# Kernel optimization log

Measured on AMD Instinct MI355X. Metric: run time of the kernel, lower is better.

Reference implementation:

```python
import jax, jax.numpy as jnp
import numpy as np

NEG_SLOPE = 0.2  # PyG GATConv default negative_slope


def gat_layer(x, edge_index, W, att_src, att_dst, bias):
    """GATConv with self-loops, concat heads. x:[N,F_in], W:[F_in,H*C]."""
    N = x.shape[0]
    H, C = att_src.shape
    loop = jnp.arange(N, dtype=edge_index.dtype)
    src = jnp.concatenate([edge_index[0], loop])  # [E+N]
    dst = jnp.concatenate([edge_index[1], loop])
    h = (x @ W).reshape(N, H, C)                  # [N,H,C]
    a_src = jnp.einsum('nhc,hc->nh', h, att_src)  # [N,H]
    a_dst = jnp.einsum('nhc,hc->nh', h, att_dst)
    e = a_src[src] + a_dst[dst]                   # [E+N,H]
    e = jnp.where(e > 0, e, NEG_SLOPE * e)        # leaky_relu
    # numerically-stable segment softmax over incoming edges of each dst node
    m = jax.ops.segment_max(e, dst, num_segments=N)           # [N,H]
    ex = jnp.exp(e - m[dst])
    denom = jax.ops.segment_sum(ex, dst, num_segments=N)      # [N,H]
    alpha = ex / (denom[dst] + 1e-16)                          # [E+N,H]
    out = jax.ops.segment_sum(h[src] * alpha[:, :, None], dst, num_segments=N)
    return out.reshape(N, H * C) + bias


def setup_inputs() -> dict:
    key = jax.random.key(0)
    ks = jax.random.split(key, 16)
    N, E, F_IN, HID, H, NCLS = 50000, 800000, 128, 64, 4, 40
    HC = H * HID
    s = 0.1
    return {
        'x': jax.random.normal(ks[0], (N, F_IN), jnp.float32),
        'edge_index': jax.random.randint(ks[1], (2, E), 0, N, jnp.int32),
        'W1': jax.random.normal(ks[2], (F_IN, HC), jnp.float32) * s,
        'att_src1': jax.random.normal(ks[3], (H, HID), jnp.float32) * s,
        'att_dst1': jax.random.normal(ks[4], (H, HID), jnp.float32) * s,
        'b1': jnp.zeros((HC,), jnp.float32),
        'W2': jax.random.normal(ks[5], (HC, HC), jnp.float32) * s,
        'att_src2': jax.random.normal(ks[6], (H, HID), jnp.float32) * s,
        'att_dst2': jax.random.normal(ks[7], (H, HID), jnp.float32) * s,
        'b2': jnp.zeros((HC,), jnp.float32),
        'fcW1': jax.random.normal(ks[8], (HC, HID), jnp.float32) * s,
        'fcb1': jnp.zeros((HID,), jnp.float32),
        'fcW2': jax.random.normal(ks[9], (HID, NCLS), jnp.float32) * s,
        'fcb2': jnp.zeros((NCLS,), jnp.float32),
    }


def reference(x, edge_index, W1, att_src1, att_dst1, b1,
              W2, att_src2, att_dst2, b2, fcW1, fcb1, fcW2, fcb2):
    h = gat_layer(x, edge_index, W1, att_src1, att_dst1, b1)
    h = jax.nn.elu(h)
    h = gat_layer(h, edge_index, W2, att_src2, att_dst2, b2)
    h = jax.nn.elu(h)
    h = jnp.maximum(h @ fcW1 + fcb1, 0.0)  # ReLU; dropout is identity in eval
    return h @ fcW2 + fcb2                 # [N, num_classes]
```

## Files before the change

### kernel.cpp

```cpp
#include <hip/hip_runtime.h>

typedef __attribute__((ext_vector_type(8))) _Float16 fp16x8;
typedef __attribute__((ext_vector_type(4))) float f32x4;
typedef unsigned int u32;

__device__ __forceinline__ float lrelu(float x) { return x > 0.f ? x : 0.2f * x; }
__device__ __forceinline__ float elu(float x) { return x > 0.f ? x : __expf(x) - 1.f; }

__device__ __forceinline__ void gl2lds16(const void* g, void* l) {
    __builtin_amdgcn_global_load_lds((const __attribute__((address_space(1))) u32*)g,
                                     (__attribute__((address_space(3))) u32*)l, 16, 0, 0);
}

__device__ __forceinline__ void t16t_body(const float* __restrict__ W, _Float16* __restrict__ T,
                                          int N, int Nreal, int t) {
    int lane = t & 63, rem = t >> 6;
    int kk = rem & 1; rem >>= 1;
    int ncg = N / 16;
    int cg = rem % ncg, kc = rem / ncg;
    int k = kc * 64 + kk * 32 + (lane >> 4) * 8;
    int n = cg * 16 + (lane & 15);
    fp16x8 o;
#pragma unroll
    for (int j = 0; j < 8; ++j)
        o[j] = (n < Nreal) ? (_Float16)W[(size_t)(k + j) * Nreal + n] : (_Float16)0.f;
    *(fp16x8*)(T + (size_t)t * 8) = o;
}

__global__ __launch_bounds__(256) void k_prep(const float* __restrict__ W1, _Float16* __restrict__ W1T,
                                              const float* __restrict__ W2, _Float16* __restrict__ W2T,
                                              const float* __restrict__ fcW1, _Float16* __restrict__ fWT,
                                              const float* __restrict__ fcW2, _Float16* __restrict__ f2T,
                                              const int* __restrict__ dst, int* __restrict__ cnt) {
    int b = blockIdx.x, tid = threadIdx.x;
    if (b < 16)      t16t_body(W1, W1T, 256, 256, b * 256 + tid);
    else if (b < 48) t16t_body(W2, W2T, 256, 256, (b - 16) * 256 + tid);
    else if (b < 56) t16t_body(fcW1, fWT, 64, 64, (b - 48) * 256 + tid);
    else if (b < 58) t16t_body(fcW2, f2T, 64, 40, (b - 56) * 256 + tid);
    else             atomicAdd(&cnt[dst[(b - 58) * 256 + tid]], 1);
}

__global__ __launch_bounds__(256) void k_scan_a(const int* __restrict__ cnt, int* __restrict__ s,
                                                int* __restrict__ partial, int N) {
    __shared__ int sh[256];
    int t = threadIdx.x, gid = blockIdx.x * 256 + t;
    sh[t] = gid < N ? cnt[gid] : 0;
    __syncthreads();
    for (int off = 1; off < 256; off <<= 1) {
        int add = (t >= off) ? sh[t - off] : 0;
        __syncthreads();
        sh[t] += add;
        __syncthreads();
    }
    if (gid < N) s[gid] = sh[t];
    if (t == 255) partial[blockIdx.x] = sh[255];
}
__global__ __launch_bounds__(256) void k_scan_bc(const int* __restrict__ s, const int* __restrict__ partial,
                                                 const int* __restrict__ cnt, int* __restrict__ row_ptr,
                                                 int* __restrict__ cursor, int* __restrict__ bcur, int N) {
    __shared__ int red[256];
    int t = threadIdx.x, bid = blockIdx.x;
    int a = 0;
    for (int i = t; i < bid; i += 256) a += partial[i];
    red[t] = a;
    __syncthreads();
    for (int off = 128; off; off >>= 1) {
        if (t < off) red[t] += red[t + off];
        __syncthreads();
    }
    int base = red[0];
    int gid = bid * 256 + t;
    if (gid >= N) return;
    int val = s[gid] + base;
    row_ptr[gid + 1] = val;
    int excl = val - cnt[gid];
    cursor[gid] = excl;
    if ((gid & 511) == 0) bcur[gid >> 9] = excl;
    if (gid == 0) row_ptr[0] = 0;
}

__global__ __launch_bounds__(256) void k_bin(const int* __restrict__ src, const int* __restrict__ dst,
                                             int* __restrict__ bcur, int2* __restrict__ pairbuf, int E) {
    __shared__ int cnt[128], gbase[128], excl[128], cur2[128], sh[128];
    __shared__ int saddr[1024];
    __shared__ int2 spair[1024];
    const int tid = threadIdx.x;
    const int eb = blockIdx.x * 1024;
    if (tid < 128) { cnt[tid] = 0; cur2[tid] = 0; }
    __syncthreads();
    int s_[4], d_[4];
#pragma unroll
    for (int j = 0; j < 4; ++j) {
        int e = eb + j * 256 + tid;
        if (e < E) {
            s_[j] = src[e]; d_[j] = dst[e];
            atomicAdd(&cnt[d_[j] >> 9], 1);
        } else d_[j] = -1;
    }
    __syncthreads();
    if (tid < 128) sh[tid] = cnt[tid];
    __syncthreads();
    for (int off = 1; off < 128; off <<= 1) {
        int add = 0;
        if (tid < 128 && tid >= off) add = sh[tid - off];
        __syncthreads();
        if (tid < 128) sh[tid] += add;
        __syncthreads();
    }
    if (tid < 128) {
        excl[tid] = sh[tid] - cnt[tid];
        if (cnt[tid] > 0) gbase[tid] = atomicAdd(&bcur[tid], cnt[tid]);
    }
    __syncthreads();
#pragma unroll
    for (int j = 0; j < 4; ++j) {
        if (d_[j] >= 0) {
            int b = d_[j] >> 9;
            int r = atomicAdd(&cur2[b], 1);
            int slot = excl[b] + r;
            spair[slot] = make_int2(s_[j], d_[j]);
            saddr[slot] = gbase[b] + r;
        }
    }
    __syncthreads();
    int tot = min(1024, E - eb);
#pragma unroll
    for (int j = 0; j < 4; ++j) {
        int slot = j * 256 + tid;
        if (slot < tot) pairbuf[saddr[slot]] = spair[slot];
    }
}

template<int KV, int NW, int ATT, int AFP32>
__device__ __forceinline__ void gemm_body(int bid,
              const _Float16* __restrict__ Ah, const float* __restrict__ Af,
              const _Float16* __restrict__ BT, _Float16* __restrict__ Chi,
              const float* __restrict__ att_s, const float* __restrict__ att_d,
              float* __restrict__ a_src, float* __restrict__ a_dst,
              int M, int Nc) {
    constexpr int NCG = NW / 16;
    constexpr int CHUNK = NW * 64;
    constexpr int FPW = (CHUNK / 512) / 8;
    __shared__ _Float16 Bs[CHUNK];
    const int m0 = bid * 128;
    const int tid = threadIdx.x;
    const int lane = tid & 63, wv = tid >> 6;
    const int r16 = lane & 15, quad = lane >> 4;
    const int arow = min(m0 + wv * 16 + r16, M - 1);

    f32x4 acc[NCG];
#pragma unroll
    for (int cg = 0; cg < NCG; ++cg) acc[cg] = (f32x4){0, 0, 0, 0};

    constexpr int NCH = KV / 64;
#pragma unroll
    for (int kc = 0; kc < NCH; ++kc) {
        if (kc) __syncthreads();
#pragma unroll
        for (int f = 0; f < FPW; ++f) {
            int fr = wv * FPW + f;
            gl2lds16(BT + (size_t)kc * CHUNK + fr * 512 + lane * 8, &Bs[fr * 512]);
        }
        fp16x8 ar[2];
        if (AFP32) {
            const float* Ap = Af + (size_t)arow * KV + kc * 64 + quad * 8;
#pragma unroll
            for (int kk = 0; kk < 2; ++kk) {
                float4 u0 = *(const float4*)(Ap + kk * 32);
                float4 u1 = *(const float4*)(Ap + kk * 32 + 4);
                fp16x8 h8;
                h8[0] = (_Float16)u0.x; h8[1] = (_Float16)u0.y;
                h8[2] = (_Float16)u0.z; h8[3] = (_Float16)u0.w;
                h8[4] = (_Float16)u1.x; h8[5] = (_Float16)u1.y;
                h8[6] = (_Float16)u1.z; h8[7] = (_Float16)u1.w;
                ar[kk] = h8;
            }
        } else {
            const _Float16* Ahp = Ah + (size_t)arow * KV + kc * 64 + quad * 8;
#pragma unroll
            for (int kk = 0; kk < 2; ++kk) ar[kk] = *(const fp16x8*)(Ahp + kk * 32);
        }
        __syncthreads();
#pragma unroll
        for (int kk = 0; kk < 2; ++kk) {
#pragma unroll
            for (int cg = 0; cg < NCG; ++cg) {
                fp16x8 bh = *(const fp16x8*)(&Bs[(cg * 2 + kk) * 512 + lane * 8]);
                acc[cg] = __builtin_amdgcn_mfma_f32_16x16x32_f16(ar[kk], bh, acc[cg], 0, 0, 0);
            }
        }
    }

    const int rbase = m0 + wv * 16 + quad * 4;

    if (ATT) {
#pragma unroll
        for (int hq = 0; hq < 4; ++hq) {
            float as[4], ad[4];
#pragma unroll
            for (int cg = 0; cg < 4; ++cg) {
                as[cg] = att_s[hq * 64 + cg * 16 + r16];
                ad[cg] = att_d[hq * 64 + cg * 16 + r16];
            }
#pragma unroll
            for (int i = 0; i < 4; ++i) {
                float ps = acc[hq * 4 + 0][i] * as[0] + acc[hq * 4 + 1][i] * as[1]
                         + acc[hq * 4 + 2][i] * as[2] + acc[hq * 4 + 3][i] * as[3];
                float pd = acc[hq * 4 + 0][i] * ad[0] + acc[hq * 4 + 1][i] * ad[1]
                         + acc[hq * 4 + 2][i] * ad[2] + acc[hq * 4 + 3][i] * ad[3];
#pragma unroll
                for (int d = 1; d < 16; d <<= 1) {
                    ps += __shfl_xor(ps, d);
                    pd += __shfl_xor(pd, d);
                }
                int r = rbase + i;
                if (r16 == 0 && r < M) {
                    a_src[(size_t)r * 4 + hq] = ps;
                    a_dst[(size_t)r * 4 + hq] = pd;
                }
            }
        }
    }

#pragma unroll
    for (int cg = 0; cg < NCG; ++cg) {
        int c = cg * 16 + r16;
        if (c >= Nc) continue;
#pragma unroll
        for (int i = 0; i < 4; ++i) {
            int r = rbase + i;
            if (r < M) Chi[(size_t)r * Nc + c] = (_Float16)acc[cg][i];
        }
    }
}

__global__ __launch_bounds__(512, 4)
void k_work1(const float* __restrict__ x, const _Float16* __restrict__ W1T,
             _Float16* __restrict__ h,
             const float* __restrict__ att_s, const float* __restrict__ att_d,
             float* __restrict__ a_src, float* __restrict__ a_dst,
             const int2* __restrict__ pairbuf,
             int* __restrict__ cursor, int* __restrict__ csr,
             int M, int E, int RB) {
    if ((int)blockIdx.x >= RB) {
        int base = (blockIdx.x - RB) * 2048;
#pragma unroll
        for (int j = 0; j < 4; ++j) {
            int i = base + j * 512 + threadIdx.x;
            if (i < E) {
                int2 p = pairbuf[i];
                int pos = atomicAdd(&cursor[p.y], 1);
                csr[pos] = p.x;
            }
        }
        return;
    }
    gemm_body<128, 256, 1, 1>(blockIdx.x, nullptr, x, W1T, h, att_s, att_d, a_src, a_dst, M, 256);
}

__global__ __launch_bounds__(512, 4)
void k_gemm2(const _Float16* __restrict__ Ah, const _Float16* __restrict__ BT,
             _Float16* __restrict__ h,
             const float* __restrict__ att_s, const float* __restrict__ att_d,
             float* __restrict__ a_src, float* __restrict__ a_dst, int M) {
    gemm_body<256, 256, 1, 0>(blockIdx.x, Ah, nullptr, BT, h, att_s, att_d, a_src, a_dst, M, 256);
}

__global__ __launch_bounds__(256, 4)
void k_fc(const _Float16* __restrict__ Ah, const _Float16* __restrict__ BT1,
          const _Float16* __restrict__ BT2, const float* __restrict__ b1,
          const float* __restrict__ b2, float* __restrict__ out, int M) {
    __shared__ _Float16 S[4096 + 64 * 72];
    const int m0 = blockIdx.x * 64;
    const int tid = threadIdx.x;
    const int lane = tid & 63, wv = tid >> 6;
    const int r16 = lane & 15, quad = lane >> 4;
    const int arow = min(m0 + wv * 16 + r16, M - 1);

    f32x4 acc[4];
#pragma unroll
    for (int cg = 0; cg < 4; ++cg) acc[cg] = (f32x4){0, 0, 0, 0};
#pragma unroll
    for (int kc = 0; kc < 4; ++kc) {
        if (kc) __syncthreads();
#pragma unroll
        for (int f = 0; f < 2; ++f) {
            int fr = wv * 2 + f;
            gl2lds16(BT1 + (size_t)kc * 4096 + fr * 512 + lane * 8, &S[fr * 512]);
        }
        fp16x8 ar[2];
        const _Float16* Ahp = Ah + (size_t)arow * 256 + kc * 64 + quad * 8;
#pragma unroll
        for (int kk = 0; kk < 2; ++kk) ar[kk] = *(const fp16x8*)(Ahp + kk * 32);
        __syncthreads();
#pragma unroll
        for (int kk = 0; kk < 2; ++kk) {
#pragma unroll
            for (int cg = 0; cg < 4; ++cg) {
                fp16x8 bh = *(const fp16x8*)(&S[(cg * 2 + kk) * 512 + lane * 8]);
                acc[cg] = __builtin_amdgcn_mfma_f32_16x16x32_f16(ar[kk], bh, acc[cg], 0, 0, 0);
            }
        }
    }
    __syncthreads();
    const int rloc = wv * 16 + quad * 4;
#pragma unroll
    for (int cg = 0; cg < 4; ++cg) {
        int c = cg * 16 + r16;
        float badd = b1[c];
#pragma unroll
        for (int i = 0; i < 4; ++i)
            S[4096 + (rloc + i) * 72 + c] = (_Float16)fmaxf(acc[cg][i] + badd, 0.f);
    }
    __syncthreads();
    const int arow2 = wv * 16 + r16;
    fp16x8 a2[2];
#pragma unroll
    for (int kk = 0; kk < 2; ++kk)
        a2[kk] = *(const fp16x8*)(&S[4096 + arow2 * 72 + kk * 32 + quad * 8]);
    f32x4 acc2[4];
#pragma unroll
    for (int cg = 0; cg < 4; ++cg) acc2[cg] = (f32x4){0, 0, 0, 0};
#pragma unroll
    for (int kk = 0; kk < 2; ++kk) {
#pragma unroll
        for (int cg = 0; cg < 4; ++cg) {
            fp16x8 bh = *(const fp16x8*)(BT2 + (cg * 2 + kk) * 512 + lane * 8);
            acc2[cg] = __builtin_amdgcn_mfma_f32_16x16x32_f16(a2[kk], bh, acc2[cg], 0, 0, 0);
        }
    }
    const int rbase = m0 + wv * 16 + quad * 4;
#pragma unroll
    for (int cg = 0; cg < 4; ++cg) {
        int c = cg * 16 + r16;
        if (c >= 40) continue;
        float badd = b2[c];
#pragma unroll
        for (int i = 0; i < 4; ++i) {
            int r = rbase + i;
            if (r < M) out[(size_t)r * 40 + c] = acc2[cg][i] + badd;
        }
    }
}

__global__ __launch_bounds__(256) void k_aggr8(const _Float16* __restrict__ h, const float* __restrict__ a_src,
                                               const float* __restrict__ a_dst, const int* __restrict__ row_ptr,
                                               const int* __restrict__ csr, const float* __restrict__ bias,
                                               _Float16* __restrict__ o_hi, int N) {
    int n = blockIdx.x * 8 + (threadIdx.x >> 5);
    if (n >= N) return;
    int cl = threadIdx.x & 31;
    int hd = cl >> 3;
    int beg = row_ptr[n], end = row_ptr[n + 1];
    float adh = a_dst[(size_t)4 * n + hd];
    const _Float16* hb = h + (size_t)cl * 8;

    float ws = __expf(lrelu(a_src[(size_t)4 * n + hd] + adh));
    fp16x8 sv = *(const fp16x8*)(hb + (size_t)n * 256);
    float acc[8];
#pragma unroll
    for (int j = 0; j < 8; ++j) acc[j] = ws * (float)sv[j];
    float dn = ws;

    int e = beg;
    for (; e + 4 <= end; e += 4) {
        int s0 = csr[e], s1 = csr[e + 1], s2 = csr[e + 2], s3 = csr[e + 3];
        float z0 = a_src[(size_t)4 * s0 + hd], z1 = a_src[(size_t)4 * s1 + hd];
        float z2 = a_src[(size_t)4 * s2 + hd], z3 = a_src[(size_t)4 * s3 + hd];
        fp16x8 v0 = *(const fp16x8*)(hb + (size_t)s0 * 256);
        fp16x8 v1 = *(const fp16x8*)(hb + (size_t)s1 * 256);
        fp16x8 v2 = *(const fp16x8*)(hb + (size_t)s2 * 256);
        fp16x8 v3 = *(const fp16x8*)(hb + (size_t)s3 * 256);
        float w0 = __expf(lrelu(z0 + adh)), w1 = __expf(lrelu(z1 + adh));
        float w2 = __expf(lrelu(z2 + adh)), w3 = __expf(lrelu(z3 + adh));
        dn += (w0 + w1) + (w2 + w3);
#pragma unroll
        for (int j = 0; j < 8; ++j)
            acc[j] += w0 * (float)v0[j] + w1 * (float)v1[j]
                    + w2 * (float)v2[j] + w3 * (float)v3[j];
    }
    for (; e + 2 <= end; e += 2) {
        int s0 = csr[e], s1 = csr[e + 1];
        float z0 = a_src[(size_t)4 * s0 + hd], z1 = a_src[(size_t)4 * s1 + hd];
        fp16x8 v0 = *(const fp16x8*)(hb + (size_t)s0 * 256);
        fp16x8 v1 = *(const fp16x8*)(hb + (size_t)s1 * 256);
        float w0 = __expf(lrelu(z0 + adh)), w1 = __expf(lrelu(z1 + adh));
        dn += w0 + w1;
#pragma unroll
        for (int j = 0; j < 8; ++j)
            acc[j] += w0 * (float)v0[j] + w1 * (float)v1[j];
    }
    if (e < end) {
        int s0 = csr[e];
        float w0 = __expf(lrelu(a_src[(size_t)4 * s0 + hd] + adh));
        fp16x8 v0 = *(const fp16x8*)(hb + (size_t)s0 * 256);
        dn += w0;
#pragma unroll
        for (int j = 0; j < 8; ++j) acc[j] += w0 * (float)v0[j];
    }

    float inv = 1.f / (dn + 1e-16f);
    float4 b0 = *(const float4*)(bias + cl * 8);
    float4 b1v = *(const float4*)(bias + cl * 8 + 4);
    fp16x8 hi;
    hi[0] = (_Float16)elu(acc[0] * inv + b0.x);
    hi[1] = (_Float16)elu(acc[1] * inv + b0.y);
    hi[2] = (_Float16)elu(acc[2] * inv + b0.z);
    hi[3] = (_Float16)elu(acc[3] * inv + b0.w);
    hi[4] = (_Float16)elu(acc[4] * inv + b1v.x);
    hi[5] = (_Float16)elu(acc[5] * inv + b1v.y);
    hi[6] = (_Float16)elu(acc[6] * inv + b1v.z);
    hi[7] = (_Float16)elu(acc[7] * inv + b1v.w);
    *(fp16x8*)(o_hi + (size_t)n * 256 + cl * 8) = hi;
}

extern "C" void kernel_launch(void* const* d_in, const int* in_sizes, int n_in,
                              void* d_out, int out_size, void* d_ws, size_t ws_size,
                              hipStream_t stream) {
    const int N = 50000, E = 800000, F_IN = 128, HC = 256, HID = 64, NCLS = 40;
    const float* x    = (const float*)d_in[0];
    const int*   ei   = (const int*)d_in[1];
    const float* W1   = (const float*)d_in[2];
    const float* as1  = (const float*)d_in[3];
    const float* ad1  = (const float*)d_in[4];
    const float* b1   = (const float*)d_in[5];
    const float* W2   = (const float*)d_in[6];
    const float* as2  = (const float*)d_in[7];
    const float* ad2  = (const float*)d_in[8];
    const float* b2   = (const float*)d_in[9];
    const float* fcW1 = (const float*)d_in[10];
    const float* fcb1 = (const float*)d_in[11];
    const float* fcW2 = (const float*)d_in[12];
    const float* fcb2 = (const float*)d_in[13];
    float* out = (float*)d_out;

    char* wp = (char*)d_ws;
    auto alloc = [&](size_t b) { char* p = wp; wp += (b + 255) & ~(size_t)255; return p; };
    _Float16* h     = (_Float16*)alloc((size_t)N * HC * 2);
    _Float16* ohi   = (_Float16*)alloc((size_t)N * HC * 2);
    float*  asrc  = (float*)alloc((size_t)N * 4 * 4);
    float*  adst  = (float*)alloc((size_t)N * 4 * 4);
    _Float16* W1T   = (_Float16*)alloc((size_t)F_IN * HC * 2);
    _Float16* W2T   = (_Float16*)alloc((size_t)HC * HC * 2);
    _Float16* fWT   = (_Float16*)alloc((size_t)HC * HID * 2);
    _Float16* f2T   = (_Float16*)alloc((size_t)HID * HID * 2);
    int* cnt     = (int*)alloc((size_t)N * 4);
    int* sbuf    = (int*)alloc((size_t)N * 4);
    int* part    = (int*)alloc(1024);
    int* row_ptr = (int*)alloc(((size_t)N + 1) * 4);
    int* cursor  = (int*)alloc((size_t)N * 4);
    int* csr     = (int*)alloc((size_t)E * 4);
    int* bcur    = (int*)alloc(128 * 4);
    int2* pairs  = (int2*)alloc((size_t)E * 8);

    const int* src = ei;
    const int* dst = ei + E;

    const int rb = (N + 127) / 128;
    const int node_blocks8 = (N + 7) / 8;
    const int bin_blocks = (E + 1023) / 1024;
    const int p2_blocks = (E + 2047) / 2048;
    const int fc_blocks = (N + 63) / 64;

    hipMemsetAsync(cnt, 0, (size_t)N * 4, stream);
    k_prep<<<3183, 256, 0, stream>>>(W1, W1T, W2, W2T, fcW1, fWT, fcW2, f2T, dst, cnt);
    int nb = (N + 255) / 256;
    k_scan_a<<<nb, 256, 0, stream>>>(cnt, sbuf, part, N);
    k_scan_bc<<<nb, 256, 0, stream>>>(sbuf, part, cnt, row_ptr, cursor, bcur, N);
    k_bin<<<bin_blocks, 256, 0, stream>>>(src, dst, bcur, pairs, E);
    k_work1<<<rb + p2_blocks, 512, 0, stream>>>(x, W1T, h, as1, ad1, asrc, adst,
                                                pairs, cursor, csr, N, E, rb);
    k_aggr8<<<node_blocks8, 256, 0, stream>>>(h, asrc, adst, row_ptr, csr, b1, ohi, N);
    k_gemm2<<<rb, 512, 0, stream>>>(ohi, W2T, h, as2, ad2, asrc, adst, N);
    k_aggr8<<<node_blocks8, 256, 0, stream>>>(h, asrc, adst, row_ptr, csr, b2, ohi, N);
    k_fc<<<fc_blocks, 256, 0, stream>>>(ohi, fWT, f2T, fcb1, fcb2, out, N);
}
```

Before: 340.2 us.

## Fuse layer-1 aggregation with layer-2 GEMM and attention projections

Replaces the separate layer-1 aggregation kernel and layer-2 GEMM with one kernel. Each block aggregates 16 destination nodes into an LDS tile, then runs MFMA against W2T and computes the attention logits in the same pass. This avoids writing the intermediate layer-1 output to global memory and reading it back, and removes one launch. The cost is small 16-row GEMM tiles that reload B from global/L2 per block, and no max-subtraction in the softmax. New a_src2/a_dst2 buffers are added and the h/ohi buffers swap roles.

```diff
diff --git a/kernel.cpp b/kernel.cpp
--- a/kernel.cpp
+++ b/kernel.cpp
@@ -258,12 +258,151 @@
     gemm_body<128, 256, 1, 1>(blockIdx.x, nullptr, x, W1T, h, att_s, att_d, a_src, a_dst, M, 256);
 }
 
-__global__ __launch_bounds__(512, 4)
-void k_gemm2(const _Float16* __restrict__ Ah, const _Float16* __restrict__ BT,
-             _Float16* __restrict__ h,
-             const float* __restrict__ att_s, const float* __restrict__ att_d,
-             float* __restrict__ a_src, float* __restrict__ a_dst, int M) {
-    gemm_body<256, 256, 1, 0>(blockIdx.x, Ah, nullptr, BT, h, att_s, att_d, a_src, a_dst, M, 256);
+#define AG2_LDA 264
+__global__ __launch_bounds__(512, 4) void k_ag2(
+        const _Float16* __restrict__ h, const float* __restrict__ a_src,
+        const float* __restrict__ a_dst, const int* __restrict__ row_ptr,
+        const int* __restrict__ csr, const float* __restrict__ bias,
+        const _Float16* __restrict__ BT,
+        const float* __restrict__ att_s, const float* __restrict__ att_d,
+        float* __restrict__ a_src2, float* __restrict__ a_dst2,
+        _Float16* __restrict__ h2, int N) {
+    __shared__ _Float16 A[16 * AG2_LDA];
+    __shared__ float psp[8][16], pdp[8][16];
+    const int tid = threadIdx.x;
+    const int n0 = blockIdx.x * 16;
+
+    {
+        int r = tid >> 5;
+        int n = min(n0 + r, N - 1);
+        int cl = tid & 31;
+        int hd = cl >> 3;
+        int beg = row_ptr[n], end = row_ptr[n + 1];
+        float adh = a_dst[(size_t)4 * n + hd];
+        const _Float16* hb = h + (size_t)cl * 8;
+
+        float ws = __expf(lrelu(a_src[(size_t)4 * n + hd] + adh));
+        fp16x8 sv = *(const fp16x8*)(hb + (size_t)n * 256);
+        float acc[8];
+#pragma unroll
+        for (int j = 0; j < 8; ++j) acc[j] = ws * (float)sv[j];
+        float dn = ws;
+
+        int e = beg;
+        for (; e + 4 <= end; e += 4) {
+            int s0 = csr[e], s1 = csr[e + 1], s2 = csr[e + 2], s3 = csr[e + 3];
+            float z0 = a_src[(size_t)4 * s0 + hd], z1 = a_src[(size_t)4 * s1 + hd];
+            float z2 = a_src[(size_t)4 * s2 + hd], z3 = a_src[(size_t)4 * s3 + hd];
+            fp16x8 v0 = *(const fp16x8*)(hb + (size_t)s0 * 256);
+            fp16x8 v1 = *(const fp16x8*)(hb + (size_t)s1 * 256);
+            fp16x8 v2 = *(const fp16x8*)(hb + (size_t)s2 * 256);
+            fp16x8 v3 = *(const fp16x8*)(hb + (size_t)s3 * 256);
+            float w0 = __expf(lrelu(z0 + adh)), w1 = __expf(lrelu(z1 + adh));
+            float w2 = __expf(lrelu(z2 + adh)), w3 = __expf(lrelu(z3 + adh));
+            dn += (w0 + w1) + (w2 + w3);
+#pragma unroll
+            for (int j = 0; j < 8; ++j)
+                acc[j] += w0 * (float)v0[j] + w1 * (float)v1[j]
+                        + w2 * (float)v2[j] + w3 * (float)v3[j];
+        }
+        for (; e + 2 <= end; e += 2) {
+            int s0 = csr[e], s1 = csr[e + 1];
+            float z0 = a_src[(size_t)4 * s0 + hd], z1 = a_src[(size_t)4 * s1 + hd];
+            fp16x8 v0 = *(const fp16x8*)(hb + (size_t)s0 * 256);
+            fp16x8 v1 = *(const fp16x8*)(hb + (size_t)s1 * 256);
+            float w0 = __expf(lrelu(z0 + adh)), w1 = __expf(lrelu(z1 + adh));
+            dn += w0 + w1;
+#pragma unroll
+            for (int j = 0; j < 8; ++j)
+                acc[j] += w0 * (float)v0[j] + w1 * (float)v1[j];
+        }
+        if (e < end) {
+            int s0 = csr[e];
+            float w0 = __expf(lrelu(a_src[(size_t)4 * s0 + hd] + adh));
+            fp16x8 v0 = *(const fp16x8*)(hb + (size_t)s0 * 256);
+            dn += w0;
+#pragma unroll
+            for (int j = 0; j < 8; ++j) acc[j] += w0 * (float)v0[j];
+        }
+
+        float inv = 1.f / (dn + 1e-16f);
+        float4 b0 = *(const float4*)(bias + cl * 8);
+        float4 b1v = *(const float4*)(bias + cl * 8 + 4);
+        fp16x8 hi;
+        hi[0] = (_Float16)elu(acc[0] * inv + b0.x);
+        hi[1] = (_Float16)elu(acc[1] * inv + b0.y);
+        hi[2] = (_Float16)elu(acc[2] * inv + b0.z);
+        hi[3] = (_Float16)elu(acc[3] * inv + b0.w);
+        hi[4] = (_Float16)elu(acc[4] * inv + b1v.x);
+        hi[5] = (_Float16)elu(acc[5] * inv + b1v.y);
+        hi[6] = (_Float16)elu(acc[6] * inv + b1v.z);
+        hi[7] = (_Float16)elu(acc[7] * inv + b1v.w);
+        *(fp16x8*)(&A[r * AG2_LDA + cl * 8]) = hi;
+    }
+    __syncthreads();
+
+    const int lane = tid & 63, wv = tid >> 6;
+    const int r16 = lane & 15, quad = lane >> 4;
+    f32x4 acc2[2];
+    acc2[0] = (f32x4){0, 0, 0, 0};
+    acc2[1] = (f32x4){0, 0, 0, 0};
+#pragma unroll
+    for (int kc = 0; kc < 4; ++kc) {
+        fp16x8 ar[2];
+#pragma unroll
+        for (int kk = 0; kk < 2; ++kk)
+            ar[kk] = *(const fp16x8*)(&A[r16 * AG2_LDA + kc * 64 + kk * 32 + quad * 8]);
+#pragma unroll
+        for (int kk = 0; kk < 2; ++kk) {
+#pragma unroll
+            for (int j = 0; j < 2; ++j) {
+                int cg = wv * 2 + j;
+                fp16x8 bh = *(const fp16x8*)(BT + ((size_t)(kc * 16 + cg) * 2 + kk) * 512 + lane * 8);
+                acc2[j] = __builtin_amdgcn_mfma_f32_16x16x32_f16(ar[kk], bh, acc2[j], 0, 0, 0);
+            }
+        }
+    }
+    {
+        float as[2], ad[2];
+#pragma unroll
+        for (int j = 0; j < 2; ++j) {
+            int c = (wv * 2 + j) * 16 + r16;
+            as[j] = att_s[c];
+            ad[j] = att_d[c];
+        }
+#pragma unroll
+        for (int i = 0; i < 4; ++i) {
+            float ps = acc2[0][i] * as[0] + acc2[1][i] * as[1];
+            float pd = acc2[0][i] * ad[0] + acc2[1][i] * ad[1];
+#pragma unroll
+            for (int d = 1; d < 16; d <<= 1) {
+                ps += __shfl_xor(ps, d);
+                pd += __shfl_xor(pd, d);
+            }
+            if (r16 == 0) {
+                psp[wv][quad * 4 + i] = ps;
+                pdp[wv][quad * 4 + i] = pd;
+            }
+        }
+    }
+#pragma unroll
+    for (int j = 0; j < 2; ++j) {
+        int c = (wv * 2 + j) * 16 + r16;
+#pragma unroll
+        for (int i = 0; i < 4; ++i) {
+            int rr = n0 + quad * 4 + i;
+            if (rr < N) h2[(size_t)rr * 256 + c] = (_Float16)acc2[j][i];
+        }
+    }
+    __syncthreads();
+    if (tid < 64) {
+        int row = tid >> 2, hq = tid & 3;
+        int rr = n0 + row;
+        if (rr < N) {
+            a_src2[(size_t)rr * 4 + hq] = psp[2 * hq][row] + psp[2 * hq + 1][row];
+            a_dst2[(size_t)rr * 4 + hq] = pdp[2 * hq][row] + pdp[2 * hq + 1][row];
+        }
+    }
 }
 
 __global__ __launch_bounds__(256, 4)
@@ -440,6 +579,8 @@
     _Float16* ohi   = (_Float16*)alloc((size_t)N * HC * 2);
     float*  asrc  = (float*)alloc((size_t)N * 4 * 4);
     float*  adst  = (float*)alloc((size_t)N * 4 * 4);
+    float*  asrc2 = (float*)alloc((size_t)N * 4 * 4);
+    float*  adst2 = (float*)alloc((size_t)N * 4 * 4);
     _Float16* W1T   = (_Float16*)alloc((size_t)F_IN * HC * 2);
     _Float16* W2T   = (_Float16*)alloc((size_t)HC * HC * 2);
     _Float16* fWT   = (_Float16*)alloc((size_t)HC * HID * 2);
@@ -458,6 +599,7 @@
 
     const int rb = (N + 127) / 128;
     const int node_blocks8 = (N + 7) / 8;
+    const int ag2_blocks = (N + 15) / 16;
     const int bin_blocks = (E + 1023) / 1024;
     const int p2_blocks = (E + 2047) / 2048;
     const int fc_blocks = (N + 63) / 64;
@@ -470,8 +612,8 @@
     k_bin<<<bin_blocks, 256, 0, stream>>>(src, dst, bcur, pairs, E);
     k_work1<<<rb + p2_blocks, 512, 0, stream>>>(x, W1T, h, as1, ad1, asrc, adst,
                                                 pairs, cursor, csr, N, E, rb);
-    k_aggr8<<<node_blocks8, 256, 0, stream>>>(h, asrc, adst, row_ptr, csr, b1, ohi, N);
-    k_gemm2<<<rb, 512, 0, stream>>>(ohi, W2T, h, as2, ad2, asrc, adst, N);
-    k_aggr8<<<node_blocks8, 256, 0, stream>>>(h, asrc, adst, row_ptr, csr, b2, ohi, N);
-    k_fc<<<fc_blocks, 256, 0, stream>>>(ohi, fWT, f2T, fcb1, fcb2, out, N);
-}
+    k_ag2<<<ag2_blocks, 512, 0, stream>>>(h, asrc, adst, row_ptr, csr, b1,
+                                          W2T, as2, ad2, asrc2, adst2, ohi, N);
+    k_aggr8<<<node_blocks8, 256, 0, stream>>>(ohi, asrc2, adst2, row_ptr, csr, b2, h, N);
+    k_fc<<<fc_blocks, 256, 0, stream>>>(h, fWT, f2T, fcb1, fcb2, out, N);
+}
```

New measurement: 328.5 us. 1.04x faster.
